# Kernel tuning notes

Hardware: AMD Instinct MI355X
Metric: run time of the kernel (lower is better)

## Reference

```python
import jax, jax.numpy as jnp
import numpy as np

FP4_LUT = jnp.array([0.0, 0.5, 1.0, 1.5, 2.0, 3.0, 4.0, 6.0], dtype=jnp.float32)
BLOCK = 16  # NVFP4 block size along in-features


def dequant_nvfp4(packed, scale, gscale):
    """packed: [K//2, N] int32 bytes (two fp4 e2m1 codes, lo nibble = even in-feature);
    scale: [K//16, N] block scales; gscale: scalar global scale.
    Returns W^T laid out [K, N] (in_features, out_features)."""
    lo = packed & 0xF
    hi = (packed >> 4) & 0xF
    codes = jnp.stack([lo, hi], axis=1).reshape(-1, packed.shape[1])  # [K, N]
    vals = jnp.where(codes >= 8, -1.0, 1.0) * FP4_LUT[codes & 7]
    K, N = vals.shape
    vals = (vals.reshape(K // BLOCK, BLOCK, N) * scale[:, None, :]).reshape(K, N)
    return vals * gscale


def setup_inputs() -> dict:
    key = jax.random.key(0)
    ks = jax.random.split(key, 6)
    E, H, I, T = 8, 2048, 4096, 1024
    hidden_states = jax.random.normal(ks[0], (E * T, H), dtype=jnp.float32)
    gate_up_packed = jax.random.randint(ks[1], (E, H // 2, 2 * I), 0, 256, dtype=jnp.int32)
    down_packed = jax.random.randint(ks[2], (E, I // 2, H), 0, 256, dtype=jnp.int32)
    # block scales: positive, e4m3-representable magnitudes
    gate_up_scale = (0.5 + jax.random.uniform(ks[3], (E, H // 16, 2 * I))) * 0.05
    down_scale = (0.5 + jax.random.uniform(ks[4], (E, I // 16, H))) * 0.05
    gate_up_gscale = jnp.float32(0.5)
    down_gscale = jnp.float32(0.5)
    return {"hidden_states": hidden_states, "gate_up_packed": gate_up_packed,
            "gate_up_scale": gate_up_scale, "gate_up_gscale": gate_up_gscale,
            "down_packed": down_packed, "down_scale": down_scale,
            "down_gscale": down_gscale}


def reference(hidden_states, gate_up_packed, gate_up_scale, gate_up_gscale,
              down_packed, down_scale, down_gscale):
    E = gate_up_packed.shape[0]
    H = hidden_states.shape[-1]
    x = hidden_states.reshape(E, -1, H)  # [E, T, H], tokens contiguous per expert

    def body(_, inp):
        xe, gup, gus, dp, ds = inp
        Wgu = dequant_nvfp4(gup, gus, gate_up_gscale)  # [H, 2I]
        Wd = dequant_nvfp4(dp, ds, down_gscale)        # [I, H]
        gu = xe @ Wgu                                   # [T, 2I]
        gate, up = jnp.split(gu, 2, axis=-1)
        inter = up * jax.nn.silu(gate)
        return None, inter @ Wd                         # [T, H]

    _, out = jax.lax.scan(body, None,
                          (x, gate_up_packed, gate_up_scale, down_packed, down_scale))
    return out.reshape(-1, H)
```

## Files before the change

kernel.cpp:

```cpp
#include <hip/hip_runtime.h>
#include <stdint.h>

#define E_ 8
#define H_ 2048
#define I_ 4096
#define T_ 1024
#define N1_ (2 * I_)

typedef unsigned short ushort_t;
typedef _Float16 half_t;
typedef __attribute__((ext_vector_type(2))) _Float16 h2;
typedef __attribute__((ext_vector_type(8))) _Float16 f16x8;
typedef __attribute__((ext_vector_type(4))) float f32x4;

__device__ __forceinline__ uint32_t pk2h(float a, float b) {
    auto r = __builtin_amdgcn_cvt_pkrtz(a, b);
    uint32_t u;
    __builtin_memcpy(&u, &r, 4);
    return u;
}

__device__ __forceinline__ h2 mk_ss(float sv) {
    half_t h = (half_t)(sv * 0.015625f);
    h2 r; r.x = h; r.y = h;
    return r;
}

__device__ __forceinline__ uint4 dq_quad(const int wt[4], h2 ss) {
    uint32_t t0 = __builtin_amdgcn_perm((uint32_t)wt[1], (uint32_t)wt[0], 0x0C0C0400u);
    uint32_t t1 = __builtin_amdgcn_perm((uint32_t)wt[3], (uint32_t)wt[2], 0x04000C0Cu);
    uint32_t w4 = t0 | t1;
    const uint32_t T_LO = 0x56545000u;
    const uint32_t T_HI = 0x5E5C5A58u;
    uint32_t selL = w4 & 0x07070707u;
    uint32_t selH = (w4 >> 4) & 0x07070707u;
    uint32_t hiL = __builtin_amdgcn_perm(T_HI, T_LO, selL) | ((w4 & 0x08080808u) << 4);
    uint32_t hiH = __builtin_amdgcn_perm(T_HI, T_LO, selH) | (w4 & 0x80808080u);
    uint32_t p0 = __builtin_amdgcn_perm(hiH, hiL, 0x040C000Cu);
    uint32_t p1 = __builtin_amdgcn_perm(hiH, hiL, 0x050C010Cu);
    uint32_t p2 = __builtin_amdgcn_perm(hiH, hiL, 0x060C020Cu);
    uint32_t p3 = __builtin_amdgcn_perm(hiH, hiL, 0x070C030Cu);
    uint4 q;
    h2 r0 = *(h2*)&p0 * ss; __builtin_memcpy(&q.x, &r0, 4);
    h2 r1 = *(h2*)&p1 * ss; __builtin_memcpy(&q.y, &r1, 4);
    h2 r2 = *(h2*)&p2 * ss; __builtin_memcpy(&q.z, &r2, 4);
    h2 r3 = *(h2*)&p3 * ss; __builtin_memcpy(&q.w, &r3, 4);
    return q;
}

__global__ __launch_bounds__(512, 4) void gemm1_kernel(
    const float* __restrict__ x,
    const int* __restrict__ gup,
    const float* __restrict__ gus,
    const float* __restrict__ gscale_p,
    ushort_t* __restrict__ inter,
    int e0) {
    __shared__ __align__(16) ushort_t As[2][256 * 40];
    __shared__ __align__(16) ushort_t Bs[2][128 * 40];

    const int tid = threadIdx.x;
    const int lane = tid & 63, wv = tid >> 6;
    const int quad = lane >> 4, c16 = lane & 15;
    const int mw = wv >> 1, nw = wv & 1;
    const int zloc = blockIdx.z, e = e0 + zloc;
    const int mBase = blockIdx.y * 256, nTile = blockIdx.x;
    const float gsc = gscale_p[0];

    const int kq = (tid >> 4) & 3;
    const int bn = (tid & 15) | ((tid >> 6) << 4);
    const int colg = nTile * 64 + (bn & 63) + ((bn >> 6) << 12);
    const int* bptr = gup + (size_t)e * (H_ / 2) * N1_ + (size_t)(kq * 4) * N1_ + colg;
    const float* sptr = gus + (size_t)e * (H_ / 16) * N1_ + (size_t)(kq >> 1) * N1_ + colg;

    const int arow = tid >> 2, seg = tid & 3;
    const float* ap = x + (size_t)(e * T_ + mBase + arow) * H_ + seg * 8;

    f32x4 accg[4][2], accu[4][2];
    const f32x4 z4 = {0.f, 0.f, 0.f, 0.f};
#pragma unroll
    for (int f = 0; f < 4; ++f)
#pragma unroll
        for (int b = 0; b < 2; ++b) { accg[f][b] = z4; accu[f][b] = z4; }

    float4 fa[4]; int wt[4]; float sv;
    fa[0] = *(const float4*)(ap);
    fa[1] = *(const float4*)(ap + 4);
    fa[2] = *(const float4*)(ap + (size_t)128 * H_);
    fa[3] = *(const float4*)(ap + (size_t)128 * H_ + 4);
#pragma unroll
    for (int i = 0; i < 4; ++i) wt[i] = bptr[(size_t)i * N1_];
    sv = sptr[0] * gsc;
    {
        uint4 d0, d1;
        d0.x = pk2h(fa[0].x, fa[0].y); d0.y = pk2h(fa[0].z, fa[0].w);
        d0.z = pk2h(fa[1].x, fa[1].y); d0.w = pk2h(fa[1].z, fa[1].w);
        d1.x = pk2h(fa[2].x, fa[2].y); d1.y = pk2h(fa[2].z, fa[2].w);
        d1.z = pk2h(fa[3].x, fa[3].y); d1.w = pk2h(fa[3].z, fa[3].w);
        *(uint4*)(&As[0][arow * 40 + seg * 8]) = d0;
        *(uint4*)(&As[0][(arow + 128) * 40 + seg * 8]) = d1;
        uint4 q = dq_quad(wt, mk_ss(sv));
        *(uint4*)(&Bs[0][bn * 40 + kq * 8]) = q;
    }
    __syncthreads();

    for (int kt = 0; kt < H_ / 32 - 1; ++kt) {
        const int cur = kt & 1, nxt = cur ^ 1;
        fa[0] = *(const float4*)(ap + (kt + 1) * 32);
        fa[1] = *(const float4*)(ap + (kt + 1) * 32 + 4);
        fa[2] = *(const float4*)(ap + (size_t)128 * H_ + (kt + 1) * 32);
        fa[3] = *(const float4*)(ap + (size_t)128 * H_ + (kt + 1) * 32 + 4);
        const int* bp = bptr + (size_t)(kt + 1) * 16 * N1_;
#pragma unroll
        for (int i = 0; i < 4; ++i) wt[i] = bp[(size_t)i * N1_];
        sv = sptr[(size_t)(kt + 1) * 2 * N1_] * gsc;

        f16x8 bg0 = *(const f16x8*)(&Bs[cur][(nw * 32 + c16) * 40 + quad * 8]);
        f16x8 bg1 = *(const f16x8*)(&Bs[cur][(nw * 32 + 16 + c16) * 40 + quad * 8]);
        f16x8 bu0 = *(const f16x8*)(&Bs[cur][(64 + nw * 32 + c16) * 40 + quad * 8]);
        f16x8 bu1 = *(const f16x8*)(&Bs[cur][(64 + nw * 32 + 16 + c16) * 40 + quad * 8]);
#pragma unroll
        for (int f = 0; f < 4; ++f) {
            f16x8 af = *(const f16x8*)(&As[cur][(mw * 64 + f * 16 + c16) * 40 + quad * 8]);
            accg[f][0] = __builtin_amdgcn_mfma_f32_16x16x32_f16(af, bg0, accg[f][0], 0, 0, 0);
            accg[f][1] = __builtin_amdgcn_mfma_f32_16x16x32_f16(af, bg1, accg[f][1], 0, 0, 0);
            accu[f][0] = __builtin_amdgcn_mfma_f32_16x16x32_f16(af, bu0, accu[f][0], 0, 0, 0);
            accu[f][1] = __builtin_amdgcn_mfma_f32_16x16x32_f16(af, bu1, accu[f][1], 0, 0, 0);
        }

        {
            uint4 d0, d1;
            d0.x = pk2h(fa[0].x, fa[0].y); d0.y = pk2h(fa[0].z, fa[0].w);
            d0.z = pk2h(fa[1].x, fa[1].y); d0.w = pk2h(fa[1].z, fa[1].w);
            d1.x = pk2h(fa[2].x, fa[2].y); d1.y = pk2h(fa[2].z, fa[2].w);
            d1.z = pk2h(fa[3].x, fa[3].y); d1.w = pk2h(fa[3].z, fa[3].w);
            *(uint4*)(&As[nxt][arow * 40 + seg * 8]) = d0;
            *(uint4*)(&As[nxt][(arow + 128) * 40 + seg * 8]) = d1;
            uint4 q = dq_quad(wt, mk_ss(sv));
            *(uint4*)(&Bs[nxt][bn * 40 + kq * 8]) = q;
        }
        __syncthreads();
    }

    {
        const int cur = (H_ / 32 - 1) & 1;
        f16x8 bg0 = *(const f16x8*)(&Bs[cur][(nw * 32 + c16) * 40 + quad * 8]);
        f16x8 bg1 = *(const f16x8*)(&Bs[cur][(nw * 32 + 16 + c16) * 40 + quad * 8]);
        f16x8 bu0 = *(const f16x8*)(&Bs[cur][(64 + nw * 32 + c16) * 40 + quad * 8]);
        f16x8 bu1 = *(const f16x8*)(&Bs[cur][(64 + nw * 32 + 16 + c16) * 40 + quad * 8]);
#pragma unroll
        for (int f = 0; f < 4; ++f) {
            f16x8 af = *(const f16x8*)(&As[cur][(mw * 64 + f * 16 + c16) * 40 + quad * 8]);
            accg[f][0] = __builtin_amdgcn_mfma_f32_16x16x32_f16(af, bg0, accg[f][0], 0, 0, 0);
            accg[f][1] = __builtin_amdgcn_mfma_f32_16x16x32_f16(af, bg1, accg[f][1], 0, 0, 0);
            accu[f][0] = __builtin_amdgcn_mfma_f32_16x16x32_f16(af, bu0, accu[f][0], 0, 0, 0);
            accu[f][1] = __builtin_amdgcn_mfma_f32_16x16x32_f16(af, bu1, accu[f][1], 0, 0, 0);
        }
    }

    ushort_t* ip = inter + (size_t)zloc * T_ * I_;
#pragma unroll
    for (int f = 0; f < 4; ++f)
#pragma unroll
        for (int b = 0; b < 2; ++b)
#pragma unroll
            for (int r = 0; r < 4; ++r) {
                int row = mBase + mw * 64 + f * 16 + quad * 4 + r;
                int col = nTile * 64 + nw * 32 + b * 16 + c16;
                float g = accg[f][b][r];
                float u = accu[f][b][r];
                float v = u * g / (1.f + __expf(-g));
                half_t hv = (half_t)v;
                ushort_t hu;
                __builtin_memcpy(&hu, &hv, 2);
                ip[(size_t)row * I_ + col] = hu;
            }
}

__global__ __launch_bounds__(512, 4) void gemm2_kernel(
    const ushort_t* __restrict__ inter,
    const int* __restrict__ dp,
    const float* __restrict__ dsc,
    const float* __restrict__ gscale_p,
    float* __restrict__ out,
    int e0) {
    __shared__ __align__(16) ushort_t As[2][256 * 40];
    __shared__ __align__(16) ushort_t Bs[2][128 * 40];

    const int tid = threadIdx.x;
    const int lane = tid & 63, wv = tid >> 6;
    const int quad = lane >> 4, c16 = lane & 15;
    const int mw = wv >> 1, nw = wv & 1;
    const int zloc = blockIdx.z, e = e0 + zloc;
    const int mBase = blockIdx.y * 256, nBase = blockIdx.x * 128;
    const float gsc = gscale_p[0];

    const int kq = (tid >> 4) & 3;
    const int bn = (tid & 15) | ((tid >> 6) << 4);
    const int col = nBase + bn;
    const int* bptr = dp + (size_t)e * (I_ / 2) * H_ + (size_t)(kq * 4) * H_ + col;
    const float* sptr = dsc + (size_t)e * (I_ / 16) * H_ + (size_t)(kq >> 1) * H_ + col;

    const int arow = tid >> 2, seg = tid & 3;
    const ushort_t* ap = inter + (size_t)(zloc * T_ + mBase + arow) * I_ + seg * 8;

    f32x4 acc[4][4];
    const f32x4 z4 = {0.f, 0.f, 0.f, 0.f};
#pragma unroll
    for (int f = 0; f < 4; ++f)
#pragma unroll
        for (int b = 0; b < 4; ++b) acc[f][b] = z4;

    uint4 va[2]; int wt[4]; float sv;
#pragma unroll
    for (int p = 0; p < 2; ++p) va[p] = *(const uint4*)(ap + (size_t)(p * 128) * I_);
#pragma unroll
    for (int i = 0; i < 4; ++i) wt[i] = bptr[(size_t)i * H_];
    sv = sptr[0] * gsc;
    {
#pragma unroll
        for (int p = 0; p < 2; ++p)
            *(uint4*)(&As[0][(arow + p * 128) * 40 + seg * 8]) = va[p];
        uint4 q = dq_quad(wt, mk_ss(sv));
        *(uint4*)(&Bs[0][bn * 40 + kq * 8]) = q;
    }
    __syncthreads();

    for (int kt = 0; kt < I_ / 32 - 1; ++kt) {
        const int cur = kt & 1, nxt = cur ^ 1;
#pragma unroll
        for (int p = 0; p < 2; ++p)
            va[p] = *(const uint4*)(ap + (size_t)(p * 128) * I_ + (kt + 1) * 32);
        const int* bp = bptr + (size_t)(kt + 1) * 16 * H_;
#pragma unroll
        for (int i = 0; i < 4; ++i) wt[i] = bp[(size_t)i * H_];
        sv = sptr[(size_t)(kt + 1) * 2 * H_] * gsc;

        f16x8 bfr[4];
#pragma unroll
        for (int b = 0; b < 4; ++b)
            bfr[b] = *(const f16x8*)(&Bs[cur][(nw * 64 + b * 16 + c16) * 40 + quad * 8]);
#pragma unroll
        for (int f = 0; f < 4; ++f) {
            f16x8 af = *(const f16x8*)(&As[cur][(mw * 64 + f * 16 + c16) * 40 + quad * 8]);
#pragma unroll
            for (int b = 0; b < 4; ++b)
                acc[f][b] = __builtin_amdgcn_mfma_f32_16x16x32_f16(af, bfr[b], acc[f][b], 0, 0, 0);
        }

#pragma unroll
        for (int p = 0; p < 2; ++p)
            *(uint4*)(&As[nxt][(arow + p * 128) * 40 + seg * 8]) = va[p];
        uint4 q = dq_quad(wt, mk_ss(sv));
        *(uint4*)(&Bs[nxt][bn * 40 + kq * 8]) = q;
        __syncthreads();
    }

    {
        const int cur = (I_ / 32 - 1) & 1;
        f16x8 bfr[4];
#pragma unroll
        for (int b = 0; b < 4; ++b)
            bfr[b] = *(const f16x8*)(&Bs[cur][(nw * 64 + b * 16 + c16) * 40 + quad * 8]);
#pragma unroll
        for (int f = 0; f < 4; ++f) {
            f16x8 af = *(const f16x8*)(&As[cur][(mw * 64 + f * 16 + c16) * 40 + quad * 8]);
#pragma unroll
            for (int b = 0; b < 4; ++b)
                acc[f][b] = __builtin_amdgcn_mfma_f32_16x16x32_f16(af, bfr[b], acc[f][b], 0, 0, 0);
        }
    }

#pragma unroll
    for (int f = 0; f < 4; ++f)
#pragma unroll
        for (int b = 0; b < 4; ++b)
#pragma unroll
            for (int r = 0; r < 4; ++r) {
                int row = mBase + mw * 64 + f * 16 + quad * 4 + r;
                int c = nBase + nw * 64 + b * 16 + c16;
                out[(size_t)(e * T_ + row) * H_ + c] = acc[f][b][r];
            }
}

extern "C" void kernel_launch(void* const* d_in, const int* in_sizes, int n_in,
                              void* d_out, int out_size, void* d_ws, size_t ws_size,
                              hipStream_t stream) {
    const float* x = (const float*)d_in[0];
    const int* gup = (const int*)d_in[1];
    const float* gus = (const float*)d_in[2];
    const float* gug = (const float*)d_in[3];
    const int* dp = (const int*)d_in[4];
    const float* dsc = (const float*)d_in[5];
    const float* dg = (const float*)d_in[6];
    float* out = (float*)d_out;
    ushort_t* inter = (ushort_t*)d_ws;

    const size_t per_e = (size_t)T_ * I_ * 2;
    int C = 8;
    if (ws_size < 8 * per_e) C = (ws_size >= 4 * per_e) ? 4 : (ws_size >= 2 * per_e) ? 2 : 1;

    for (int e0 = 0; e0 < E_; e0 += C) {
        gemm1_kernel<<<dim3(I_ / 64, T_ / 256, C), 512, 0, stream>>>(x, gup, gus, gug, inter, e0);
        gemm2_kernel<<<dim3(H_ / 128, T_ / 256, C), 512, 0, stream>>>(inter, dp, dsc, dg, out, e0);
    }
}
```

Measured before the change: 970.5 us.

## Pre-pack FP4 weights and fp16 activations into workspace, unroll pipeline by two

Adds pre-pass kernels that compact the int32-per-byte FP4 weights into dense 32-bit words (four bytes per word) and convert x to fp16 in the workspace. The GEMM kernels then load one word instead of four strided ints and half the activation bytes. The main loops are restructured into an explicitly two-stage register prefetch unrolled by two. The pre-passes read all the original weights each call and add extra launches and workspace use, and mode selection depends on the workspace size.

```diff
diff --git a/kernel.cpp b/kernel.cpp
--- a/kernel.cpp
+++ b/kernel.cpp
@@ -26,10 +26,13 @@
     return r;
 }
 
-__device__ __forceinline__ uint4 dq_quad(const int wt[4], h2 ss) {
-    uint32_t t0 = __builtin_amdgcn_perm((uint32_t)wt[1], (uint32_t)wt[0], 0x0C0C0400u);
-    uint32_t t1 = __builtin_amdgcn_perm((uint32_t)wt[3], (uint32_t)wt[2], 0x04000C0Cu);
-    uint32_t w4 = t0 | t1;
+__device__ __forceinline__ unsigned gather4(const int* wtv) {
+    unsigned t0 = __builtin_amdgcn_perm((unsigned)wtv[1], (unsigned)wtv[0], 0x0C0C0400u);
+    unsigned t1 = __builtin_amdgcn_perm((unsigned)wtv[3], (unsigned)wtv[2], 0x04000C0Cu);
+    return t0 | t1;
+}
+
+__device__ __forceinline__ uint4 dq4(unsigned w4, h2 ss) {
     const uint32_t T_LO = 0x56545000u;
     const uint32_t T_HI = 0x5E5C5A58u;
     uint32_t selL = w4 & 0x07070707u;
@@ -48,13 +51,44 @@
     return q;
 }
 
+template<int R4, int NC>
+__global__ __launch_bounds__(256) void pack_w_kernel(const int* __restrict__ src,
+                                                     unsigned* __restrict__ dst) {
+    const size_t total = (size_t)E_ * R4 * NC;
+    const size_t stride = (size_t)gridDim.x * 256;
+    for (size_t i = (size_t)blockIdx.x * 256 + threadIdx.x; i < total; i += stride) {
+        size_t e = i / ((size_t)R4 * NC);
+        size_t r4n = i - e * ((size_t)R4 * NC);
+        size_t r4 = r4n / NC, n = r4n - r4 * NC;
+        const int* s = src + ((e * R4 + r4) * 4) * (size_t)NC + n;
+        unsigned w0 = (unsigned)s[0], w1 = (unsigned)s[NC];
+        unsigned w2 = (unsigned)s[2 * (size_t)NC], w3 = (unsigned)s[3 * (size_t)NC];
+        unsigned t0 = __builtin_amdgcn_perm(w1, w0, 0x0C0C0400u);
+        unsigned t1 = __builtin_amdgcn_perm(w3, w2, 0x04000C0Cu);
+        dst[i] = t0 | t1;
+    }
+}
+
+__global__ __launch_bounds__(256) void pack_x_kernel(const float* __restrict__ src,
+                                                     ushort_t* __restrict__ dst) {
+    const size_t total8 = (size_t)E_ * T_ * H_ / 8;
+    const size_t stride = (size_t)gridDim.x * 256;
+    for (size_t i = (size_t)blockIdx.x * 256 + threadIdx.x; i < total8; i += stride) {
+        const float4 a = *(const float4*)(src + i * 8);
+        const float4 b = *(const float4*)(src + i * 8 + 4);
+        uint4 d;
+        d.x = pk2h(a.x, a.y); d.y = pk2h(a.z, a.w);
+        d.z = pk2h(b.x, b.y); d.w = pk2h(b.z, b.w);
+        *(uint4*)(dst + i * 8) = d;
+    }
+}
+
+template<int MODE>
 __global__ __launch_bounds__(512, 4) void gemm1_kernel(
-    const float* __restrict__ x,
-    const int* __restrict__ gup,
-    const float* __restrict__ gus,
-    const float* __restrict__ gscale_p,
-    ushort_t* __restrict__ inter,
-    int e0) {
+    const float* __restrict__ x, const ushort_t* __restrict__ xh,
+    const int* __restrict__ gup, const unsigned* __restrict__ gupc,
+    const float* __restrict__ gus, const float* __restrict__ gscale_p,
+    ushort_t* __restrict__ inter, int e0) {
     __shared__ __align__(16) ushort_t As[2][256 * 40];
     __shared__ __align__(16) ushort_t Bs[2][128 * 40];
 
@@ -70,10 +104,12 @@
     const int bn = (tid & 15) | ((tid >> 6) << 4);
     const int colg = nTile * 64 + (bn & 63) + ((bn >> 6) << 12);
     const int* bptr = gup + (size_t)e * (H_ / 2) * N1_ + (size_t)(kq * 4) * N1_ + colg;
+    const unsigned* bptrc = gupc + (size_t)e * (H_ / 8) * N1_ + (size_t)kq * N1_ + colg;
     const float* sptr = gus + (size_t)e * (H_ / 16) * N1_ + (size_t)(kq >> 1) * N1_ + colg;
 
     const int arow = tid >> 2, seg = tid & 3;
     const float* ap = x + (size_t)(e * T_ + mBase + arow) * H_ + seg * 8;
+    const ushort_t* aph = xh + (size_t)(e * T_ + mBase + arow) * H_ + seg * 8;
 
     f32x4 accg[4][2], accu[4][2];
     const f32x4 z4 = {0.f, 0.f, 0.f, 0.f};
@@ -82,80 +118,78 @@
 #pragma unroll
         for (int b = 0; b < 2; ++b) { accg[f][b] = z4; accu[f][b] = z4; }
 
-    float4 fa[4]; int wt[4]; float sv;
-    fa[0] = *(const float4*)(ap);
-    fa[1] = *(const float4*)(ap + 4);
-    fa[2] = *(const float4*)(ap + (size_t)128 * H_);
-    fa[3] = *(const float4*)(ap + (size_t)128 * H_ + 4);
-#pragma unroll
-    for (int i = 0; i < 4; ++i) wt[i] = bptr[(size_t)i * N1_];
-    sv = sptr[0] * gsc;
-    {
-        uint4 d0, d1;
-        d0.x = pk2h(fa[0].x, fa[0].y); d0.y = pk2h(fa[0].z, fa[0].w);
-        d0.z = pk2h(fa[1].x, fa[1].y); d0.w = pk2h(fa[1].z, fa[1].w);
-        d1.x = pk2h(fa[2].x, fa[2].y); d1.y = pk2h(fa[2].z, fa[2].w);
-        d1.z = pk2h(fa[3].x, fa[3].y); d1.w = pk2h(fa[3].z, fa[3].w);
-        *(uint4*)(&As[0][arow * 40 + seg * 8]) = d0;
-        *(uint4*)(&As[0][(arow + 128) * 40 + seg * 8]) = d1;
-        uint4 q = dq_quad(wt, mk_ss(sv));
-        *(uint4*)(&Bs[0][bn * 40 + kq * 8]) = q;
-    }
+    float4 fa[2][4]; uint4 va[2][2]; int wt[2][4]; unsigned bw[2]; float sv[2];
+
+#define G1_LOAD(b, t) do { \
+    if constexpr (MODE == 2) { \
+        va[b][0] = *(const uint4*)(aph + (size_t)(t) * 32); \
+        va[b][1] = *(const uint4*)(aph + (size_t)128 * H_ + (size_t)(t) * 32); \
+    } else { \
+        fa[b][0] = *(const float4*)(ap + (size_t)(t) * 32); \
+        fa[b][1] = *(const float4*)(ap + (size_t)(t) * 32 + 4); \
+        fa[b][2] = *(const float4*)(ap + (size_t)128 * H_ + (size_t)(t) * 32); \
+        fa[b][3] = *(const float4*)(ap + (size_t)128 * H_ + (size_t)(t) * 32 + 4); \
+    } \
+    if constexpr (MODE >= 1) { bw[b] = bptrc[(size_t)(t) * 4 * N1_]; } \
+    else { \
+        const int* bp_ = bptr + (size_t)(t) * 16 * N1_; \
+        wt[b][0] = bp_[0]; wt[b][1] = bp_[(size_t)N1_]; \
+        wt[b][2] = bp_[(size_t)2 * N1_]; wt[b][3] = bp_[(size_t)3 * N1_]; \
+    } \
+    sv[b] = sptr[(size_t)(t) * 2 * N1_] * gsc; \
+} while (0)
+
+#define G1_STAGE(b, L) do { \
+    if constexpr (MODE == 2) { \
+        *(uint4*)(&As[L][arow * 40 + seg * 8]) = va[b][0]; \
+        *(uint4*)(&As[L][(arow + 128) * 40 + seg * 8]) = va[b][1]; \
+    } else { \
+        uint4 d0_, d1_; \
+        d0_.x = pk2h(fa[b][0].x, fa[b][0].y); d0_.y = pk2h(fa[b][0].z, fa[b][0].w); \
+        d0_.z = pk2h(fa[b][1].x, fa[b][1].y); d0_.w = pk2h(fa[b][1].z, fa[b][1].w); \
+        d1_.x = pk2h(fa[b][2].x, fa[b][2].y); d1_.y = pk2h(fa[b][2].z, fa[b][2].w); \
+        d1_.z = pk2h(fa[b][3].x, fa[b][3].y); d1_.w = pk2h(fa[b][3].z, fa[b][3].w); \
+        *(uint4*)(&As[L][arow * 40 + seg * 8]) = d0_; \
+        *(uint4*)(&As[L][(arow + 128) * 40 + seg * 8]) = d1_; \
+    } \
+    unsigned w4_; \
+    if constexpr (MODE >= 1) w4_ = bw[b]; else w4_ = gather4(wt[b]); \
+    uint4 q_ = dq4(w4_, mk_ss(sv[b])); \
+    *(uint4*)(&Bs[L][bn * 40 + kq * 8]) = q_; \
+} while (0)
+
+#define G1_CONSUME(L) do { \
+    f16x8 bg0 = *(const f16x8*)(&Bs[L][(nw * 32 + c16) * 40 + quad * 8]); \
+    f16x8 bg1 = *(const f16x8*)(&Bs[L][(nw * 32 + 16 + c16) * 40 + quad * 8]); \
+    f16x8 bu0 = *(const f16x8*)(&Bs[L][(64 + nw * 32 + c16) * 40 + quad * 8]); \
+    f16x8 bu1 = *(const f16x8*)(&Bs[L][(64 + nw * 32 + 16 + c16) * 40 + quad * 8]); \
+    _Pragma("unroll") \
+    for (int f = 0; f < 4; ++f) { \
+        f16x8 af = *(const f16x8*)(&As[L][(mw * 64 + f * 16 + c16) * 40 + quad * 8]); \
+        accg[f][0] = __builtin_amdgcn_mfma_f32_16x16x32_f16(af, bg0, accg[f][0], 0, 0, 0); \
+        accg[f][1] = __builtin_amdgcn_mfma_f32_16x16x32_f16(af, bg1, accg[f][1], 0, 0, 0); \
+        accu[f][0] = __builtin_amdgcn_mfma_f32_16x16x32_f16(af, bu0, accu[f][0], 0, 0, 0); \
+        accu[f][1] = __builtin_amdgcn_mfma_f32_16x16x32_f16(af, bu1, accu[f][1], 0, 0, 0); \
+    } \
+} while (0)
+
+    const int NT = H_ / 32;
+    G1_LOAD(0, 0);
+    G1_LOAD(1, 1);
+    G1_STAGE(0, 0);
     __syncthreads();
-
-    for (int kt = 0; kt < H_ / 32 - 1; ++kt) {
-        const int cur = kt & 1, nxt = cur ^ 1;
-        fa[0] = *(const float4*)(ap + (kt + 1) * 32);
-        fa[1] = *(const float4*)(ap + (kt + 1) * 32 + 4);
-        fa[2] = *(const float4*)(ap + (size_t)128 * H_ + (kt + 1) * 32);
-        fa[3] = *(const float4*)(ap + (size_t)128 * H_ + (kt + 1) * 32 + 4);
-        const int* bp = bptr + (size_t)(kt + 1) * 16 * N1_;
-#pragma unroll
-        for (int i = 0; i < 4; ++i) wt[i] = bp[(size_t)i * N1_];
-        sv = sptr[(size_t)(kt + 1) * 2 * N1_] * gsc;
-
-        f16x8 bg0 = *(const f16x8*)(&Bs[cur][(nw * 32 + c16) * 40 + quad * 8]);
-        f16x8 bg1 = *(const f16x8*)(&Bs[cur][(nw * 32 + 16 + c16) * 40 + quad * 8]);
-        f16x8 bu0 = *(const f16x8*)(&Bs[cur][(64 + nw * 32 + c16) * 40 + quad * 8]);
-        f16x8 bu1 = *(const f16x8*)(&Bs[cur][(64 + nw * 32 + 16 + c16) * 40 + quad * 8]);
-#pragma unroll
-        for (int f = 0; f < 4; ++f) {
-            f16x8 af = *(const f16x8*)(&As[cur][(mw * 64 + f * 16 + c16) * 40 + quad * 8]);
-            accg[f][0] = __builtin_amdgcn_mfma_f32_16x16x32_f16(af, bg0, accg[f][0], 0, 0, 0);
-            accg[f][1] = __builtin_amdgcn_mfma_f32_16x16x32_f16(af, bg1, accg[f][1], 0, 0, 0);
-            accu[f][0] = __builtin_amdgcn_mfma_f32_16x16x32_f16(af, bu0, accu[f][0], 0, 0, 0);
-            accu[f][1] = __builtin_amdgcn_mfma_f32_16x16x32_f16(af, bu1, accu[f][1], 0, 0, 0);
-        }
-
-        {
-            uint4 d0, d1;
-            d0.x = pk2h(fa[0].x, fa[0].y); d0.y = pk2h(fa[0].z, fa[0].w);
-            d0.z = pk2h(fa[1].x, fa[1].y); d0.w = pk2h(fa[1].z, fa[1].w);
-            d1.x = pk2h(fa[2].x, fa[2].y); d1.y = pk2h(fa[2].z, fa[2].w);
-            d1.z = pk2h(fa[3].x, fa[3].y); d1.w = pk2h(fa[3].z, fa[3].w);
-            *(uint4*)(&As[nxt][arow * 40 + seg * 8]) = d0;
-            *(uint4*)(&As[nxt][(arow + 128) * 40 + seg * 8]) = d1;
-            uint4 q = dq_quad(wt, mk_ss(sv));
-            *(uint4*)(&Bs[nxt][bn * 40 + kq * 8]) = q;
-        }
+    for (int kt = 0; kt < NT; kt += 2) {
+        if (kt + 2 < NT) G1_LOAD(0, kt + 2);
+        G1_CONSUME(0);
+        G1_STAGE(1, 1);
         __syncthreads();
-    }
-
-    {
-        const int cur = (H_ / 32 - 1) & 1;
-        f16x8 bg0 = *(const f16x8*)(&Bs[cur][(nw * 32 + c16) * 40 + quad * 8]);
-        f16x8 bg1 = *(const f16x8*)(&Bs[cur][(nw * 32 + 16 + c16) * 40 + quad * 8]);
-        f16x8 bu0 = *(const f16x8*)(&Bs[cur][(64 + nw * 32 + c16) * 40 + quad * 8]);
-        f16x8 bu1 = *(const f16x8*)(&Bs[cur][(64 + nw * 32 + 16 + c16) * 40 + quad * 8]);
-#pragma unroll
-        for (int f = 0; f < 4; ++f) {
-            f16x8 af = *(const f16x8*)(&As[cur][(mw * 64 + f * 16 + c16) * 40 + quad * 8]);
-            accg[f][0] = __builtin_amdgcn_mfma_f32_16x16x32_f16(af, bg0, accg[f][0], 0, 0, 0);
-            accg[f][1] = __builtin_amdgcn_mfma_f32_16x16x32_f16(af, bg1, accg[f][1], 0, 0, 0);
-            accu[f][0] = __builtin_amdgcn_mfma_f32_16x16x32_f16(af, bu0, accu[f][0], 0, 0, 0);
-            accu[f][1] = __builtin_amdgcn_mfma_f32_16x16x32_f16(af, bu1, accu[f][1], 0, 0, 0);
-        }
-    }
+        if (kt + 3 < NT) G1_LOAD(1, kt + 3);
+        G1_CONSUME(1);
+        if (kt + 2 < NT) { G1_STAGE(0, 0); __syncthreads(); }
+    }
+#undef G1_LOAD
+#undef G1_STAGE
+#undef G1_CONSUME
 
     ushort_t* ip = inter + (size_t)zloc * T_ * I_;
 #pragma unroll
@@ -176,13 +210,12 @@
             }
 }
 
+template<int MODE>
 __global__ __launch_bounds__(512, 4) void gemm2_kernel(
     const ushort_t* __restrict__ inter,
-    const int* __restrict__ dp,
-    const float* __restrict__ dsc,
-    const float* __restrict__ gscale_p,
-    float* __restrict__ out,
-    int e0) {
+    const int* __restrict__ dp, const unsigned* __restrict__ dpc,
+    const float* __restrict__ dsc, const float* __restrict__ gscale_p,
+    float* __restrict__ out, int e0) {
     __shared__ __align__(16) ushort_t As[2][256 * 40];
     __shared__ __align__(16) ushort_t Bs[2][128 * 40];
 
@@ -198,6 +231,7 @@
     const int bn = (tid & 15) | ((tid >> 6) << 4);
     const int col = nBase + bn;
     const int* bptr = dp + (size_t)e * (I_ / 2) * H_ + (size_t)(kq * 4) * H_ + col;
+    const unsigned* bptrc = dpc + (size_t)e * (I_ / 8) * H_ + (size_t)kq * H_ + col;
     const float* sptr = dsc + (size_t)e * (I_ / 16) * H_ + (size_t)(kq >> 1) * H_ + col;
 
     const int arow = tid >> 2, seg = tid & 3;
@@ -210,65 +244,60 @@
 #pragma unroll
         for (int b = 0; b < 4; ++b) acc[f][b] = z4;
 
-    uint4 va[2]; int wt[4]; float sv;
-#pragma unroll
-    for (int p = 0; p < 2; ++p) va[p] = *(const uint4*)(ap + (size_t)(p * 128) * I_);
-#pragma unroll
-    for (int i = 0; i < 4; ++i) wt[i] = bptr[(size_t)i * H_];
-    sv = sptr[0] * gsc;
-    {
-#pragma unroll
-        for (int p = 0; p < 2; ++p)
-            *(uint4*)(&As[0][(arow + p * 128) * 40 + seg * 8]) = va[p];
-        uint4 q = dq_quad(wt, mk_ss(sv));
-        *(uint4*)(&Bs[0][bn * 40 + kq * 8]) = q;
-    }
+    uint4 va[2][2]; int wt[2][4]; unsigned bw[2]; float sv[2];
+
+#define G2_LOAD(b, t) do { \
+    va[b][0] = *(const uint4*)(ap + (size_t)(t) * 32); \
+    va[b][1] = *(const uint4*)(ap + (size_t)128 * I_ + (size_t)(t) * 32); \
+    if constexpr (MODE >= 1) { bw[b] = bptrc[(size_t)(t) * 4 * H_]; } \
+    else { \
+        const int* bp_ = bptr + (size_t)(t) * 16 * H_; \
+        wt[b][0] = bp_[0]; wt[b][1] = bp_[(size_t)H_]; \
+        wt[b][2] = bp_[(size_t)2 * H_]; wt[b][3] = bp_[(size_t)3 * H_]; \
+    } \
+    sv[b] = sptr[(size_t)(t) * 2 * H_] * gsc; \
+} while (0)
+
+#define G2_STAGE(b, L) do { \
+    *(uint4*)(&As[L][arow * 40 + seg * 8]) = va[b][0]; \
+    *(uint4*)(&As[L][(arow + 128) * 40 + seg * 8]) = va[b][1]; \
+    unsigned w4_; \
+    if constexpr (MODE >= 1) w4_ = bw[b]; else w4_ = gather4(wt[b]); \
+    uint4 q_ = dq4(w4_, mk_ss(sv[b])); \
+    *(uint4*)(&Bs[L][bn * 40 + kq * 8]) = q_; \
+} while (0)
+
+#define G2_CONSUME(L) do { \
+    f16x8 bfr[4]; \
+    _Pragma("unroll") \
+    for (int b = 0; b < 4; ++b) \
+        bfr[b] = *(const f16x8*)(&Bs[L][(nw * 64 + b * 16 + c16) * 40 + quad * 8]); \
+    _Pragma("unroll") \
+    for (int f = 0; f < 4; ++f) { \
+        f16x8 af = *(const f16x8*)(&As[L][(mw * 64 + f * 16 + c16) * 40 + quad * 8]); \
+        _Pragma("unroll") \
+        for (int b = 0; b < 4; ++b) \
+            acc[f][b] = __builtin_amdgcn_mfma_f32_16x16x32_f16(af, bfr[b], acc[f][b], 0, 0, 0); \
+    } \
+} while (0)
+
+    const int NT = I_ / 32;
+    G2_LOAD(0, 0);
+    G2_LOAD(1, 1);
+    G2_STAGE(0, 0);
     __syncthreads();
-
-    for (int kt = 0; kt < I_ / 32 - 1; ++kt) {
-        const int cur = kt & 1, nxt = cur ^ 1;
-#pragma unroll
-        for (int p = 0; p < 2; ++p)
-            va[p] = *(const uint4*)(ap + (size_t)(p * 128) * I_ + (kt + 1) * 32);
-        const int* bp = bptr + (size_t)(kt + 1) * 16 * H_;
-#pragma unroll
-        for (int i = 0; i < 4; ++i) wt[i] = bp[(size_t)i * H_];
-        sv = sptr[(size_t)(kt + 1) * 2 * H_] * gsc;
-
-        f16x8 bfr[4];
-#pragma unroll
-        for (int b = 0; b < 4; ++b)
-            bfr[b] = *(const f16x8*)(&Bs[cur][(nw * 64 + b * 16 + c16) * 40 + quad * 8]);
-#pragma unroll
-        for (int f = 0; f < 4; ++f) {
-            f16x8 af = *(const f16x8*)(&As[cur][(mw * 64 + f * 16 + c16) * 40 + quad * 8]);
-#pragma unroll
-            for (int b = 0; b < 4; ++b)
-                acc[f][b] = __builtin_amdgcn_mfma_f32_16x16x32_f16(af, bfr[b], acc[f][b], 0, 0, 0);
-        }
-
-#pragma unroll
-        for (int p = 0; p < 2; ++p)
-            *(uint4*)(&As[nxt][(arow + p * 128) * 40 + seg * 8]) = va[p];
-        uint4 q = dq_quad(wt, mk_ss(sv));
-        *(uint4*)(&Bs[nxt][bn * 40 + kq * 8]) = q;
+    for (int kt = 0; kt < NT; kt += 2) {
+        if (kt + 2 < NT) G2_LOAD(0, kt + 2);
+        G2_CONSUME(0);
+        G2_STAGE(1, 1);
         __syncthreads();
-    }
-
-    {
-        const int cur = (I_ / 32 - 1) & 1;
-        f16x8 bfr[4];
-#pragma unroll
-        for (int b = 0; b < 4; ++b)
-            bfr[b] = *(const f16x8*)(&Bs[cur][(nw * 64 + b * 16 + c16) * 40 + quad * 8]);
-#pragma unroll
-        for (int f = 0; f < 4; ++f) {
-            f16x8 af = *(const f16x8*)(&As[cur][(mw * 64 + f * 16 + c16) * 40 + quad * 8]);
-#pragma unroll
-            for (int b = 0; b < 4; ++b)
-                acc[f][b] = __builtin_amdgcn_mfma_f32_16x16x32_f16(af, bfr[b], acc[f][b], 0, 0, 0);
-        }
-    }
+        if (kt + 3 < NT) G2_LOAD(1, kt + 3);
+        G2_CONSUME(1);
+        if (kt + 2 < NT) { G2_STAGE(0, 0); __syncthreads(); }
+    }
+#undef G2_LOAD
+#undef G2_STAGE
+#undef G2_CONSUME
 
 #pragma unroll
     for (int f = 0; f < 4; ++f)
@@ -293,14 +322,50 @@
     const float* dsc = (const float*)d_in[5];
     const float* dg = (const float*)d_in[6];
     float* out = (float*)d_out;
-    ushort_t* inter = (ushort_t*)d_ws;
+    uint8_t* wsb = (uint8_t*)d_ws;
 
     const size_t per_e = (size_t)T_ * I_ * 2;
-    int C = 8;
-    if (ws_size < 8 * per_e) C = (ws_size >= 4 * per_e) ? 4 : (ws_size >= 2 * per_e) ? 2 : 1;
+    const size_t wg_b = (size_t)E_ * (H_ / 8) * N1_ * 4;
+    const size_t wd_b = (size_t)E_ * (I_ / 8) * H_ * 4;
+    const size_t xh_b = (size_t)E_ * T_ * H_ * 2;
+    const size_t tail_end = ws_size & ~(size_t)15;
+
+    int mode; size_t resv;
+    if (tail_end >= wg_b + wd_b + xh_b + per_e) { mode = 2; resv = wg_b + wd_b + xh_b; }
+    else if (tail_end >= wg_b + wd_b + per_e)   { mode = 1; resv = wg_b + wd_b; }
+    else                                        { mode = 0; resv = 0; }
+    const size_t avail = tail_end - resv;
+    int C = avail >= 8 * per_e ? 8 : avail >= 4 * per_e ? 4 : avail >= 2 * per_e ? 2 : 1;
+
+    ushort_t* inter = (ushort_t*)wsb;
+    unsigned* wgc = (unsigned*)(wsb + tail_end - resv);
+    unsigned* wdc = (unsigned*)(wsb + tail_end - resv + wg_b);
+    ushort_t* xhp = (ushort_t*)(wsb + tail_end - resv + wg_b + wd_b);
+    const ushort_t* xh_arg = (mode == 2) ? (const ushort_t*)xhp : (const ushort_t*)wsb;
+    const unsigned* wgc_arg = (mode >= 1) ? (const unsigned*)wgc : (const unsigned*)wsb;
+    const unsigned* wdc_arg = (mode >= 1) ? (const unsigned*)wdc : (const unsigned*)wsb;
+
+    if (mode >= 1) {
+        pack_w_kernel<H_ / 8, N1_><<<2048, 256, 0, stream>>>(gup, wgc);
+        pack_w_kernel<I_ / 8, H_><<<2048, 256, 0, stream>>>(dp, wdc);
+    }
+    if (mode == 2) pack_x_kernel<<<2048, 256, 0, stream>>>(x, xhp);
 
     for (int e0 = 0; e0 < E_; e0 += C) {
-        gemm1_kernel<<<dim3(I_ / 64, T_ / 256, C), 512, 0, stream>>>(x, gup, gus, gug, inter, e0);
-        gemm2_kernel<<<dim3(H_ / 128, T_ / 256, C), 512, 0, stream>>>(inter, dp, dsc, dg, out, e0);
-    }
-}
+        dim3 g1(I_ / 64, T_ / 256, C), g2(H_ / 128, T_ / 256, C);
+        switch (mode) {
+            case 2:
+                gemm1_kernel<2><<<g1, 512, 0, stream>>>(x, xh_arg, gup, wgc_arg, gus, gug, inter, e0);
+                gemm2_kernel<1><<<g2, 512, 0, stream>>>(inter, dp, wdc_arg, dsc, dg, out, e0);
+                break;
+            case 1:
+                gemm1_kernel<1><<<g1, 512, 0, stream>>>(x, xh_arg, gup, wgc_arg, gus, gug, inter, e0);
+                gemm2_kernel<1><<<g2, 512, 0, stream>>>(inter, dp, wdc_arg, dsc, dg, out, e0);
+                break;
+            default:
+                gemm1_kernel<0><<<g1, 512, 0, stream>>>(x, xh_arg, gup, wgc_arg, gus, gug, inter, e0);
+                gemm2_kernel<0><<<g2, 512, 0, stream>>>(inter, dp, wdc_arg, dsc, dg, out, e0);
+                break;
+        }
+    }
+}
```

New measurement: 1.666 ms. 1.72x slower.
